# Kernel tuning notes

Hardware: AMD Instinct MI355X
Metric: run time of the kernel (lower is better)

## Reference

```python
import jax, jax.numpy as jnp
import numpy as np

NU = 200000  # num_users
NI = 200000  # num_items
D = 128      # d_model
B = 4096     # interaction batch


def setup_inputs() -> dict:
    key = jax.random.key(0)
    ks = jax.random.split(key, 24)
    f = lambda k, s, sc=1.0: (jax.random.normal(k, s, dtype=jnp.float32) * sc)
    s = 1.0 / np.sqrt(D)
    return {
        "user_id": jax.random.randint(ks[0], (B,), 0, NU),
        "prev_item_id": jax.random.randint(ks[1], (B,), 0, NI),
        "item_id": jax.random.randint(ks[2], (B,), 0, NI),
        "time_since_prev_item": jax.random.uniform(ks[3], (B, 1), dtype=jnp.float32),
        "time_since_prev_user": jax.random.uniform(ks[4], (B, 1), dtype=jnp.float32),
        "dynamic_user_emb": f(ks[5], (NU, D), 0.1),
        "dynamic_item_emb": f(ks[6], (NI, D), 0.1),
        "is_user_new": jnp.ones((NU, 1), dtype=jnp.float32),
        "is_item_new": jnp.ones((NI, 1), dtype=jnp.float32),
        "static_user_W": f(ks[7], (NU, D)),
        "static_item_W": f(ks[8], (NI, D)),
        "initial_user_emb": f(ks[9], (1, D)),
        "initial_item_emb": f(ks[10], (1, D)),
        "user_Wih": f(ks[11], (D, D + 1), s),
        "user_Whh": f(ks[12], (D, D), s),
        "user_bih": f(ks[13], (D,), s),
        "user_bhh": f(ks[14], (D,), s),
        "item_Wih": f(ks[15], (D, D + 1), s),
        "item_Whh": f(ks[16], (D, D), s),
        "item_bih": f(ks[17], (D,), s),
        "item_bhh": f(ks[18], (D,), s),
        "pred_W": f(ks[19], (2 * D, 4 * D), 1.0 / np.sqrt(4 * D)),
        "pred_b": f(ks[20], (2 * D,), 1.0 / np.sqrt(4 * D)),
        "td_W": f(ks[21], (D, 1)),
        "td_b": f(ks[22], (D,)),
    }


def _rnn_cell(x, h, Wih, Whh, bih, bhh):
    # torch.nn.RNNCell: tanh(x @ Wih^T + bih + h @ Whh^T + bhh)
    return jnp.tanh(x @ Wih.T + bih + h @ Whh.T + bhh)


def reference(user_id, prev_item_id, item_id, time_since_prev_item, time_since_prev_user,
              dynamic_user_emb, dynamic_item_emb, is_user_new, is_item_new,
              static_user_W, static_item_W, initial_user_emb, initial_item_emb,
              user_Wih, user_Whh, user_bih, user_bhh,
              item_Wih, item_Whh, item_bih, item_bhh,
              pred_W, pred_b, td_W, td_b):
    # gather dynamic embeddings (fall back to initial emb for new entities)
    user_emb = is_user_new[user_id] * initial_user_emb + dynamic_user_emb[user_id]
    item_emb = is_item_new[item_id] * initial_item_emb + dynamic_item_emb[item_id]
    prev_item_emb = is_item_new[prev_item_id] * initial_item_emb + dynamic_item_emb[prev_item_id]
    static_user_emb = static_user_W[user_id]
    static_item_emb = static_item_W[item_id]
    prev_static_item_emb = static_item_W[prev_item_id]

    # time projection + prediction head
    user_proj = user_emb * (1.0 + time_since_prev_item @ td_W.T + td_b)
    item_pred = jnp.concatenate(
        [user_proj, prev_item_emb, prev_static_item_emb, static_user_emb], axis=1) @ pred_W.T + pred_b
    item_target = jnp.concatenate([item_emb, static_item_emb], axis=1)

    # RNNCell updates
    updated_user_emb = _rnn_cell(jnp.concatenate([item_emb, time_since_prev_item], axis=1),
                                 user_emb, user_Wih, user_Whh, user_bih, user_bhh)
    updated_item_emb = _rnn_cell(jnp.concatenate([user_emb, time_since_prev_user], axis=1),
                                 item_emb, item_Wih, item_Whh, item_bih, item_bhh)

    # scatter back into persistent buffers (detached, as in torch)
    new_dyn_user = dynamic_user_emb.at[user_id].set(jax.lax.stop_gradient(updated_user_emb))
    new_dyn_item = dynamic_item_emb.at[item_id].set(jax.lax.stop_gradient(updated_item_emb))
    new_is_user_new = is_user_new.at[user_id].set(0.0)
    new_is_item_new = is_item_new.at[item_id].set(0.0)

    return (item_pred, item_target, updated_user_emb, user_emb, updated_item_emb, item_emb,
            new_dyn_user, new_dyn_item, new_is_user_new, new_is_item_new)
```

## Files before the change

kernel.cpp:

```cpp
#include <hip/hip_runtime.h>
#include <hip/hip_bf16.h>

#define NU 200000
#define NI 200000
#define D 128
#define BATCH 4096

typedef __bf16 bf16x8 __attribute__((ext_vector_type(8)));
typedef float f32x4 __attribute__((ext_vector_type(4)));

__global__ __launch_bounds__(256) void prep_kernel(
    const float* __restrict__ predW,
    const float* __restrict__ uWih, const float* __restrict__ uWhh,
    const float* __restrict__ iWih, const float* __restrict__ iWhh,
    const float* __restrict__ ubih, const float* __restrict__ ubhh,
    const float* __restrict__ ibih, const float* __restrict__ ibhh,
    const int* __restrict__ uid, const int* __restrict__ iid,
    __hip_bfloat16* __restrict__ wPred,
    __hip_bfloat16* __restrict__ wU, __hip_bfloat16* __restrict__ wI,
    float* __restrict__ biasU, float* __restrict__ biasI,
    int* __restrict__ lastU, int* __restrict__ lastI)
{
    int idx = blockIdx.x * 256 + threadIdx.x;
    if (idx < 131072) {
        wPred[idx] = __float2bfloat16(predW[idx]);
        return;
    }
    idx -= 131072;
    if (idx < 73728) {
        int z = idx / 36864;
        int r = idx - z * 36864;
        int j = r / 288, k = r - (r / 288) * 288;
        const float* Wih = z ? iWih : uWih;
        const float* Whh = z ? iWhh : uWhh;
        float v = 0.0f;
        if (k < 129)      v = Wih[j * 129 + k];
        else if (k < 257) v = Whh[j * 128 + (k - 129)];
        __hip_bfloat16* W = z ? wI : wU;
        W[j * 288 + k] = __float2bfloat16(v);
        return;
    }
    idx -= 73728;
    if (idx < 128) { biasU[idx] = ubih[idx] + ubhh[idx]; return; }
    idx -= 128;
    if (idx < 128) { biasI[idx] = ibih[idx] + ibhh[idx]; return; }
    idx -= 128;
    if (idx < BATCH) { atomicMax(&lastU[uid[idx]], idx); return; }
    idx -= BATCH;
    if (idx < BATCH) { atomicMax(&lastI[iid[idx]], idx); return; }
}

__global__ __launch_bounds__(128) void gather_kernel(
    const int* __restrict__ uid, const int* __restrict__ pid,
    const int* __restrict__ iid,
    const float* __restrict__ t_i, const float* __restrict__ t_u,
    const float* __restrict__ dynU, const float* __restrict__ dynI,
    const float* __restrict__ isU, const float* __restrict__ isI,
    const float* __restrict__ statU, const float* __restrict__ statI,
    const float* __restrict__ initU, const float* __restrict__ initI,
    const float* __restrict__ tdW, const float* __restrict__ tdb,
    float* __restrict__ o_user_emb, float* __restrict__ o_item_emb,
    float* __restrict__ o_target,
    __hip_bfloat16* __restrict__ xpred,
    __hip_bfloat16* __restrict__ xhU, __hip_bfloat16* __restrict__ xhI)
{
    int b = blockIdx.x;
    int d = threadIdx.x;
    int u = uid[b], i = iid[b], p = pid[b];
    float fu = isU[u], fi = isI[i], fp = isI[p];
    float iu = initU[d], ii = initI[d];
    float ue = fu * iu + dynU[(size_t)u * D + d];
    float ie = fi * ii + dynI[(size_t)i * D + d];
    float pe = fp * ii + dynI[(size_t)p * D + d];
    float su = statU[(size_t)u * D + d];
    float si = statI[(size_t)i * D + d];
    float sp = statI[(size_t)p * D + d];
    float ti = t_i[b], tu = t_u[b];

    o_user_emb[b * D + d] = ue;
    o_item_emb[b * D + d] = ie;
    o_target[b * 256 + d] = ie;
    o_target[b * 256 + 128 + d] = si;

    float proj = ue * (1.0f + ti * tdW[d] + tdb[d]);

    __hip_bfloat16* xp = xpred + (size_t)b * 512;
    xp[d]       = __float2bfloat16(proj);
    xp[128 + d] = __float2bfloat16(pe);
    xp[256 + d] = __float2bfloat16(sp);
    xp[384 + d] = __float2bfloat16(su);

    __hip_bfloat16* xu = xhU + (size_t)b * 288;
    xu[d]       = __float2bfloat16(ie);
    xu[129 + d] = __float2bfloat16(ue);
    __hip_bfloat16* xi = xhI + (size_t)b * 288;
    xi[d]       = __float2bfloat16(ue);
    xi[129 + d] = __float2bfloat16(ie);
    if (d == 0) {
        xu[128] = __float2bfloat16(ti);
        xi[128] = __float2bfloat16(tu);
    }
    if (d < 31) {
        xu[257 + d] = __float2bfloat16(0.0f);
        xi[257 + d] = __float2bfloat16(0.0f);
    }
}

__global__ __launch_bounds__(256) void gemm_pred(
    const __hip_bfloat16* __restrict__ A,
    const __hip_bfloat16* __restrict__ W,
    const float* __restrict__ bias,
    float* __restrict__ out)
{
    const int K = 512;
    int m0 = blockIdx.x * 64;
    int n0 = blockIdx.y * 64;
    int tid = threadIdx.x;
    int wave = tid >> 6;
    int lane = tid & 63;
    int quad = lane >> 4;
    int l15 = lane & 15;
    int row_a = m0 + wave * 16 + l15;

    f32x4 acc[4] = {};
    const __hip_bfloat16* Arow = A + (size_t)row_a * K;
    for (int k0 = 0; k0 < K; k0 += 32) {
        bf16x8 a = *reinterpret_cast<const bf16x8*>(Arow + k0 + quad * 8);
#pragma unroll
        for (int ct = 0; ct < 4; ++ct) {
            int rw = n0 + ct * 16 + l15;
            bf16x8 bb = *reinterpret_cast<const bf16x8*>(W + (size_t)rw * K + k0 + quad * 8);
            acc[ct] = __builtin_amdgcn_mfma_f32_16x16x32_bf16(a, bb, acc[ct], 0, 0, 0);
        }
    }
    int orow = m0 + wave * 16 + quad * 4;
#pragma unroll
    for (int ct = 0; ct < 4; ++ct) {
        int col = n0 + ct * 16 + l15;
        float bcol = bias[col];
#pragma unroll
        for (int r = 0; r < 4; ++r) {
            out[(size_t)(orow + r) * 256 + col] = acc[ct][r] + bcol;
        }
    }
}

__global__ __launch_bounds__(256) void gemm_cell(
    const __hip_bfloat16* __restrict__ A0, const __hip_bfloat16* __restrict__ A1,
    const __hip_bfloat16* __restrict__ W0, const __hip_bfloat16* __restrict__ W1,
    const float* __restrict__ b0, const float* __restrict__ b1,
    const int* __restrict__ ids0, const int* __restrict__ ids1,
    const int* __restrict__ last0, const int* __restrict__ last1,
    float* __restrict__ outB0, float* __restrict__ outB1,
    float* __restrict__ outD0, float* __restrict__ outD1)
{
    const int K = 288;
    int z = blockIdx.z;
    const __hip_bfloat16* A = z ? A1 : A0;
    const __hip_bfloat16* W = z ? W1 : W0;
    const float* bias = z ? b1 : b0;
    const int* ids  = z ? ids1 : ids0;
    const int* last = z ? last1 : last0;
    float* outB = z ? outB1 : outB0;
    float* outD = z ? outD1 : outD0;

    int m0 = blockIdx.x * 64;
    int n0 = blockIdx.y * 64;
    int tid = threadIdx.x;
    int wave = tid >> 6;
    int lane = tid & 63;
    int quad = lane >> 4;
    int l15 = lane & 15;
    int row_a = m0 + wave * 16 + l15;

    f32x4 acc[4] = {};
    const __hip_bfloat16* Arow = A + (size_t)row_a * K;
    for (int k0 = 0; k0 < K; k0 += 32) {
        bf16x8 a = *reinterpret_cast<const bf16x8*>(Arow + k0 + quad * 8);
#pragma unroll
        for (int ct = 0; ct < 4; ++ct) {
            int rw = n0 + ct * 16 + l15;
            bf16x8 bb = *reinterpret_cast<const bf16x8*>(W + (size_t)rw * K + k0 + quad * 8);
            acc[ct] = __builtin_amdgcn_mfma_f32_16x16x32_bf16(a, bb, acc[ct], 0, 0, 0);
        }
    }
    int orow = m0 + wave * 16 + quad * 4;
#pragma unroll
    for (int ct = 0; ct < 4; ++ct) {
        int col = n0 + ct * 16 + l15;
        float bcol = bias[col];
#pragma unroll
        for (int r = 0; r < 4; ++r) {
            int row = orow + r;
            float v = tanhf(acc[ct][r] + bcol);
            outB[(size_t)row * D + col] = v;
            int id = ids[row];
            if (last[id] == row) {
                outD[(size_t)id * D + col] = v;
            }
        }
    }
}

__global__ __launch_bounds__(256) void copy_kernel(
    const float4* __restrict__ dynU, const float4* __restrict__ dynI,
    const float* __restrict__ isU, const float* __restrict__ isI,
    const int* __restrict__ lastU, const int* __restrict__ lastI,
    float4* __restrict__ oDynU, float4* __restrict__ oDynI,
    float* __restrict__ oIsU, float* __restrict__ oIsI)
{
    long long idx = (long long)blockIdx.x * 256 + threadIdx.x;
    const long long NU4 = (long long)NU * 32;
    const long long NI4 = (long long)NI * 32;
    if (idx < NU4) {
        int row = (int)(idx >> 5);
        if (lastU[row] < 0) oDynU[idx] = dynU[idx];
        return;
    }
    idx -= NU4;
    if (idx < NI4) {
        int row = (int)(idx >> 5);
        if (lastI[row] < 0) oDynI[idx] = dynI[idx];
        return;
    }
    idx -= NI4;
    if (idx < NU) { oIsU[idx] = (lastU[idx] >= 0) ? 0.0f : isU[idx]; return; }
    idx -= NU;
    if (idx < NI) { oIsI[idx] = (lastI[idx] >= 0) ? 0.0f : isI[idx]; return; }
}

extern "C" void kernel_launch(void* const* d_in, const int* in_sizes, int n_in,
                              void* d_out, int out_size, void* d_ws, size_t ws_size,
                              hipStream_t stream) {
    const int*   uid   = (const int*)d_in[0];
    const int*   pid   = (const int*)d_in[1];
    const int*   iid   = (const int*)d_in[2];
    const float* t_i   = (const float*)d_in[3];
    const float* t_u   = (const float*)d_in[4];
    const float* dynU  = (const float*)d_in[5];
    const float* dynI  = (const float*)d_in[6];
    const float* isU   = (const float*)d_in[7];
    const float* isI   = (const float*)d_in[8];
    const float* statU = (const float*)d_in[9];
    const float* statI = (const float*)d_in[10];
    const float* initU = (const float*)d_in[11];
    const float* initI = (const float*)d_in[12];
    const float* uWih  = (const float*)d_in[13];
    const float* uWhh  = (const float*)d_in[14];
    const float* ubih  = (const float*)d_in[15];
    const float* ubhh  = (const float*)d_in[16];
    const float* iWih  = (const float*)d_in[17];
    const float* iWhh  = (const float*)d_in[18];
    const float* ibih  = (const float*)d_in[19];
    const float* ibhh  = (const float*)d_in[20];
    const float* predW = (const float*)d_in[21];
    const float* predb = (const float*)d_in[22];
    const float* tdW   = (const float*)d_in[23];
    const float* tdb   = (const float*)d_in[24];

    float* out = (float*)d_out;
    float* o_pred     = out;
    float* o_target   = out + 1048576;
    float* o_updU     = out + 2097152;
    float* o_userEmb  = out + 2621440;
    float* o_updI     = out + 3145728;
    float* o_itemEmb  = out + 3670016;
    float* o_dynU     = out + 4194304;
    float* o_dynI     = out + 29794304;
    float* o_isU      = out + 55394304;
    float* o_isI      = out + 55594304;

    char* ws = (char*)d_ws;
    int* lastU = (int*)ws;
    int* lastI = lastU + NU;
    __hip_bfloat16* xpred = (__hip_bfloat16*)(ws + 1600000);
    __hip_bfloat16* xhU   = (__hip_bfloat16*)(ws + 5794304);
    __hip_bfloat16* xhI   = (__hip_bfloat16*)(ws + 8153600);
    __hip_bfloat16* wPred = (__hip_bfloat16*)(ws + 10512896);
    __hip_bfloat16* wU    = (__hip_bfloat16*)(ws + 10775040);
    __hip_bfloat16* wI    = (__hip_bfloat16*)(ws + 10848768);
    float* biasU = (float*)(ws + 10922496);
    float* biasI = (float*)(ws + 10923008);

    hipMemsetAsync(lastU, 0xFF, (size_t)(NU + NI) * sizeof(int), stream);

    {
        int total = 131072 + 73728 + 256 + 2 * BATCH;
        int blocks = (total + 255) / 256;
        prep_kernel<<<blocks, 256, 0, stream>>>(
            predW, uWih, uWhh, iWih, iWhh, ubih, ubhh, ibih, ibhh,
            uid, iid, wPred, wU, wI, biasU, biasI, lastU, lastI);
    }

    gather_kernel<<<BATCH, 128, 0, stream>>>(
        uid, pid, iid, t_i, t_u, dynU, dynI, isU, isI, statU, statI,
        initU, initI, tdW, tdb, o_userEmb, o_itemEmb, o_target,
        xpred, xhU, xhI);

    gemm_pred<<<dim3(BATCH / 64, 4), 256, 0, stream>>>(xpred, wPred, predb, o_pred);

    gemm_cell<<<dim3(BATCH / 64, 2, 2), 256, 0, stream>>>(
        xhU, xhI, wU, wI, biasU, biasI, uid, iid, lastU, lastI,
        o_updU, o_updI, o_dynU, o_dynI);

    {
        long long total = (long long)NU * 32 + (long long)NI * 32 + NU + NI;
        int blocks = (int)((total + 255) / 256);
        copy_kernel<<<blocks, 256, 0, stream>>>(
            (const float4*)dynU, (const float4*)dynI, isU, isI, lastU, lastI,
            (float4*)o_dynU, (float4*)o_dynI, o_isU, o_isI);
    }
}
```

Baseline: 504.0 us.

## Fuse gather with unconditional table copy and merge GEMMs, scatter after copy

The full dynamic-embedding and is_new table copy now happens unconditionally inside the vectorized gather kernel, with no per-row lastU/lastI check. The two GEMM kernels merge into one launch that scatters updated rows and zeroes the is_new flags after the copy has finished. This cuts two launches and the dependent reads of the last-index arrays during the large copy. The gather now uses float4 loads and packed bf16 stores, and the cell input layout is reordered (h first, then x and time) so the vector stores stay aligned. The risk is that the scattered rows are written twice, and correctness relies on stream ordering between the copy and the GEMM.

```diff
diff --git a/kernel.cpp b/kernel.cpp
--- a/kernel.cpp
+++ b/kernel.cpp
@@ -8,6 +8,20 @@
 
 typedef __bf16 bf16x8 __attribute__((ext_vector_type(8)));
 typedef float f32x4 __attribute__((ext_vector_type(4)));
+
+__device__ __forceinline__ void store_bf16x4(__hip_bfloat16* p, float4 v) {
+    union { __hip_bfloat16 h[4]; uint2 u; } pk;
+    pk.h[0] = __float2bfloat16(v.x);
+    pk.h[1] = __float2bfloat16(v.y);
+    pk.h[2] = __float2bfloat16(v.z);
+    pk.h[3] = __float2bfloat16(v.w);
+    *reinterpret_cast<uint2*>(p) = pk.u;
+}
+
+__device__ __forceinline__ float4 f4_fma(float s, float4 a, float4 b) {
+    return make_float4(fmaf(s, a.x, b.x), fmaf(s, a.y, b.y),
+                       fmaf(s, a.z, b.z), fmaf(s, a.w, b.w));
+}
 
 __global__ __launch_bounds__(256) void prep_kernel(
     const float* __restrict__ predW,
@@ -34,8 +48,8 @@
         const float* Wih = z ? iWih : uWih;
         const float* Whh = z ? iWhh : uWhh;
         float v = 0.0f;
-        if (k < 129)      v = Wih[j * 129 + k];
-        else if (k < 257) v = Whh[j * 128 + (k - 129)];
+        if (k < 128)      v = Whh[j * 128 + k];
+        else if (k < 257) v = Wih[j * 129 + (k - 128)];
         __hip_bfloat16* W = z ? wI : wU;
         W[j * 288 + k] = __float2bfloat16(v);
         return;
@@ -50,7 +64,7 @@
     if (idx < BATCH) { atomicMax(&lastI[iid[idx]], idx); return; }
 }
 
-__global__ __launch_bounds__(128) void gather_kernel(
+__global__ __launch_bounds__(256) void gather_copy_kernel(
     const int* __restrict__ uid, const int* __restrict__ pid,
     const int* __restrict__ iid,
     const float* __restrict__ t_i, const float* __restrict__ t_u,
@@ -62,171 +76,162 @@
     float* __restrict__ o_user_emb, float* __restrict__ o_item_emb,
     float* __restrict__ o_target,
     __hip_bfloat16* __restrict__ xpred,
-    __hip_bfloat16* __restrict__ xhU, __hip_bfloat16* __restrict__ xhI)
+    __hip_bfloat16* __restrict__ xhU, __hip_bfloat16* __restrict__ xhI,
+    float4* __restrict__ oDynU, float4* __restrict__ oDynI,
+    float4* __restrict__ oIsU, float4* __restrict__ oIsI)
 {
-    int b = blockIdx.x;
-    int d = threadIdx.x;
-    int u = uid[b], i = iid[b], p = pid[b];
-    float fu = isU[u], fi = isI[i], fp = isI[p];
-    float iu = initU[d], ii = initI[d];
-    float ue = fu * iu + dynU[(size_t)u * D + d];
-    float ie = fi * ii + dynI[(size_t)i * D + d];
-    float pe = fp * ii + dynI[(size_t)p * D + d];
-    float su = statU[(size_t)u * D + d];
-    float si = statI[(size_t)i * D + d];
-    float sp = statI[(size_t)p * D + d];
-    float ti = t_i[b], tu = t_u[b];
-
-    o_user_emb[b * D + d] = ue;
-    o_item_emb[b * D + d] = ie;
-    o_target[b * 256 + d] = ie;
-    o_target[b * 256 + 128 + d] = si;
-
-    float proj = ue * (1.0f + ti * tdW[d] + tdb[d]);
-
-    __hip_bfloat16* xp = xpred + (size_t)b * 512;
-    xp[d]       = __float2bfloat16(proj);
-    xp[128 + d] = __float2bfloat16(pe);
-    xp[256 + d] = __float2bfloat16(sp);
-    xp[384 + d] = __float2bfloat16(su);
-
-    __hip_bfloat16* xu = xhU + (size_t)b * 288;
-    xu[d]       = __float2bfloat16(ie);
-    xu[129 + d] = __float2bfloat16(ue);
-    __hip_bfloat16* xi = xhI + (size_t)b * 288;
-    xi[d]       = __float2bfloat16(ue);
-    xi[129 + d] = __float2bfloat16(ie);
-    if (d == 0) {
-        xu[128] = __float2bfloat16(ti);
-        xi[128] = __float2bfloat16(tu);
+    long long idx = (long long)blockIdx.x * 256 + threadIdx.x;
+    if (idx < 131072) {
+        int b = (int)(idx >> 5);
+        int g = (int)(idx & 31);
+        const float4* dU4 = (const float4*)dynU;
+        const float4* dI4 = (const float4*)dynI;
+        const float4* sU4 = (const float4*)statU;
+        const float4* sI4 = (const float4*)statI;
+
+        int u = uid[b], i = iid[b], p = pid[b];
+        float fu = isU[u], fi = isI[i], fp = isI[p];
+        float ti = t_i[b], tu = t_u[b];
+
+        float4 iu = ((const float4*)initU)[g];
+        float4 ii = ((const float4*)initI)[g];
+        float4 ue = f4_fma(fu, iu, dU4[(size_t)u * 32 + g]);
+        float4 ie = f4_fma(fi, ii, dI4[(size_t)i * 32 + g]);
+        float4 pe = f4_fma(fp, ii, dI4[(size_t)p * 32 + g]);
+        float4 su = sU4[(size_t)u * 32 + g];
+        float4 si = sI4[(size_t)i * 32 + g];
+        float4 sp = sI4[(size_t)p * 32 + g];
+        float4 tw = ((const float4*)tdW)[g];
+        float4 tb = ((const float4*)tdb)[g];
+
+        ((float4*)o_user_emb)[(size_t)b * 32 + g] = ue;
+        ((float4*)o_item_emb)[(size_t)b * 32 + g] = ie;
+        ((float4*)o_target)[(size_t)b * 64 + g] = ie;
+        ((float4*)o_target)[(size_t)b * 64 + 32 + g] = si;
+
+        float4 f = f4_fma(ti, tw, tb);
+        float4 proj = make_float4(ue.x * (1.0f + f.x), ue.y * (1.0f + f.y),
+                                  ue.z * (1.0f + f.z), ue.w * (1.0f + f.w));
+
+        __hip_bfloat16* xp = xpred + (size_t)b * 512;
+        store_bf16x4(xp + 4 * g, proj);
+        store_bf16x4(xp + 128 + 4 * g, pe);
+        store_bf16x4(xp + 256 + 4 * g, sp);
+        store_bf16x4(xp + 384 + 4 * g, su);
+
+        __hip_bfloat16* xu = xhU + (size_t)b * 288;
+        store_bf16x4(xu + 4 * g, ue);
+        store_bf16x4(xu + 128 + 4 * g, ie);
+        __hip_bfloat16* xi = xhI + (size_t)b * 288;
+        store_bf16x4(xi + 4 * g, ie);
+        store_bf16x4(xi + 128 + 4 * g, ue);
+        if (g < 8) {
+            float4 zu = make_float4(g == 0 ? ti : 0.0f, 0.0f, 0.0f, 0.0f);
+            float4 zi = make_float4(g == 0 ? tu : 0.0f, 0.0f, 0.0f, 0.0f);
+            store_bf16x4(xu + 256 + 4 * g, zu);
+            store_bf16x4(xi + 256 + 4 * g, zi);
+        }
+        return;
     }
-    if (d < 31) {
-        xu[257 + d] = __float2bfloat16(0.0f);
-        xi[257 + d] = __float2bfloat16(0.0f);
-    }
-}
-
-__global__ __launch_bounds__(256) void gemm_pred(
-    const __hip_bfloat16* __restrict__ A,
-    const __hip_bfloat16* __restrict__ W,
-    const float* __restrict__ bias,
-    float* __restrict__ out)
+    idx -= 131072;
+    if (idx < 6400000) { oDynU[idx] = ((const float4*)dynU)[idx]; return; }
+    idx -= 6400000;
+    if (idx < 6400000) { oDynI[idx] = ((const float4*)dynI)[idx]; return; }
+    idx -= 6400000;
+    if (idx < 50000) { oIsU[idx] = ((const float4*)isU)[idx]; return; }
+    idx -= 50000;
+    if (idx < 50000) { oIsI[idx] = ((const float4*)isI)[idx]; return; }
+}
+
+__global__ __launch_bounds__(256) void gemm_fused(
+    const __hip_bfloat16* __restrict__ xpred,
+    const __hip_bfloat16* __restrict__ wPred,
+    const float* __restrict__ predb, float* __restrict__ o_pred,
+    const __hip_bfloat16* __restrict__ xhU, const __hip_bfloat16* __restrict__ xhI,
+    const __hip_bfloat16* __restrict__ wU, const __hip_bfloat16* __restrict__ wI,
+    const float* __restrict__ biasU, const float* __restrict__ biasI,
+    const int* __restrict__ uid, const int* __restrict__ iid,
+    const int* __restrict__ lastU, const int* __restrict__ lastI,
+    float* __restrict__ o_updU, float* __restrict__ o_updI,
+    float* __restrict__ o_dynU, float* __restrict__ o_dynI,
+    float* __restrict__ o_isU, float* __restrict__ o_isI)
 {
-    const int K = 512;
-    int m0 = blockIdx.x * 64;
-    int n0 = blockIdx.y * 64;
+    int bx = blockIdx.x;
     int tid = threadIdx.x;
-    int wave = tid >> 6;
-    int lane = tid & 63;
-    int quad = lane >> 4;
-    int l15 = lane & 15;
-    int row_a = m0 + wave * 16 + l15;
-
-    f32x4 acc[4] = {};
-    const __hip_bfloat16* Arow = A + (size_t)row_a * K;
-    for (int k0 = 0; k0 < K; k0 += 32) {
-        bf16x8 a = *reinterpret_cast<const bf16x8*>(Arow + k0 + quad * 8);
+    int wave = tid >> 6, lane = tid & 63, quad = lane >> 4, l15 = lane & 15;
+
+    if (bx < 256) {
+        const int K = 512;
+        int m0 = (bx & 63) * 64, n0 = (bx >> 6) * 64;
+        f32x4 acc[4] = {};
+        const __hip_bfloat16* Arow = xpred + (size_t)(m0 + wave * 16 + l15) * K;
+        for (int k0 = 0; k0 < K; k0 += 32) {
+            bf16x8 a = *reinterpret_cast<const bf16x8*>(Arow + k0 + quad * 8);
+#pragma unroll
+            for (int ct = 0; ct < 4; ++ct) {
+                bf16x8 b = *reinterpret_cast<const bf16x8*>(
+                    wPred + (size_t)(n0 + ct * 16 + l15) * K + k0 + quad * 8);
+                acc[ct] = __builtin_amdgcn_mfma_f32_16x16x32_bf16(a, b, acc[ct], 0, 0, 0);
+            }
+        }
+        int orow = m0 + wave * 16 + quad * 4;
 #pragma unroll
         for (int ct = 0; ct < 4; ++ct) {
-            int rw = n0 + ct * 16 + l15;
-            bf16x8 bb = *reinterpret_cast<const bf16x8*>(W + (size_t)rw * K + k0 + quad * 8);
-            acc[ct] = __builtin_amdgcn_mfma_f32_16x16x32_bf16(a, bb, acc[ct], 0, 0, 0);
-        }
-    }
-    int orow = m0 + wave * 16 + quad * 4;
-#pragma unroll
-    for (int ct = 0; ct < 4; ++ct) {
-        int col = n0 + ct * 16 + l15;
-        float bcol = bias[col];
-#pragma unroll
-        for (int r = 0; r < 4; ++r) {
-            out[(size_t)(orow + r) * 256 + col] = acc[ct][r] + bcol;
-        }
-    }
-}
-
-__global__ __launch_bounds__(256) void gemm_cell(
-    const __hip_bfloat16* __restrict__ A0, const __hip_bfloat16* __restrict__ A1,
-    const __hip_bfloat16* __restrict__ W0, const __hip_bfloat16* __restrict__ W1,
-    const float* __restrict__ b0, const float* __restrict__ b1,
-    const int* __restrict__ ids0, const int* __restrict__ ids1,
-    const int* __restrict__ last0, const int* __restrict__ last1,
-    float* __restrict__ outB0, float* __restrict__ outB1,
-    float* __restrict__ outD0, float* __restrict__ outD1)
-{
-    const int K = 288;
-    int z = blockIdx.z;
-    const __hip_bfloat16* A = z ? A1 : A0;
-    const __hip_bfloat16* W = z ? W1 : W0;
-    const float* bias = z ? b1 : b0;
-    const int* ids  = z ? ids1 : ids0;
-    const int* last = z ? last1 : last0;
-    float* outB = z ? outB1 : outB0;
-    float* outD = z ? outD1 : outD0;
-
-    int m0 = blockIdx.x * 64;
-    int n0 = blockIdx.y * 64;
-    int tid = threadIdx.x;
-    int wave = tid >> 6;
-    int lane = tid & 63;
-    int quad = lane >> 4;
-    int l15 = lane & 15;
-    int row_a = m0 + wave * 16 + l15;
-
-    f32x4 acc[4] = {};
-    const __hip_bfloat16* Arow = A + (size_t)row_a * K;
-    for (int k0 = 0; k0 < K; k0 += 32) {
-        bf16x8 a = *reinterpret_cast<const bf16x8*>(Arow + k0 + quad * 8);
-#pragma unroll
-        for (int ct = 0; ct < 4; ++ct) {
-            int rw = n0 + ct * 16 + l15;
-            bf16x8 bb = *reinterpret_cast<const bf16x8*>(W + (size_t)rw * K + k0 + quad * 8);
-            acc[ct] = __builtin_amdgcn_mfma_f32_16x16x32_bf16(a, bb, acc[ct], 0, 0, 0);
-        }
-    }
-    int orow = m0 + wave * 16 + quad * 4;
-#pragma unroll
-    for (int ct = 0; ct < 4; ++ct) {
-        int col = n0 + ct * 16 + l15;
-        float bcol = bias[col];
+            int col = n0 + ct * 16 + l15;
+            float bc = predb[col];
+#pragma unroll
+            for (int r = 0; r < 4; ++r)
+                o_pred[(size_t)(orow + r) * 256 + col] = acc[ct][r] + bc;
+        }
+    } else {
+        bx -= 256;
+        int z = bx >> 7; bx &= 127;
+        int m0 = (bx & 63) * 64, n0 = (bx >> 6) * 64;
+        const __hip_bfloat16* A = z ? xhI : xhU;
+        const __hip_bfloat16* W = z ? wI : wU;
+        const float* bias = z ? biasI : biasU;
+        const int* ids  = z ? iid : uid;
+        const int* last = z ? lastI : lastU;
+        float* outB = z ? o_updI : o_updU;
+        float* outD = z ? o_dynI : o_dynU;
+        float* oIs  = z ? o_isI  : o_isU;
+
+        const int K = 288;
+        f32x4 acc[4] = {};
+        const __hip_bfloat16* Arow = A + (size_t)(m0 + wave * 16 + l15) * K;
+        for (int k0 = 0; k0 < K; k0 += 32) {
+            bf16x8 a = *reinterpret_cast<const bf16x8*>(Arow + k0 + quad * 8);
+#pragma unroll
+            for (int ct = 0; ct < 4; ++ct) {
+                bf16x8 b = *reinterpret_cast<const bf16x8*>(
+                    W + (size_t)(n0 + ct * 16 + l15) * K + k0 + quad * 8);
+                acc[ct] = __builtin_amdgcn_mfma_f32_16x16x32_bf16(a, b, acc[ct], 0, 0, 0);
+            }
+        }
+        int orow = m0 + wave * 16 + quad * 4;
+        int rid[4], win[4];
 #pragma unroll
         for (int r = 0; r < 4; ++r) {
             int row = orow + r;
-            float v = tanhf(acc[ct][r] + bcol);
-            outB[(size_t)row * D + col] = v;
-            int id = ids[row];
-            if (last[id] == row) {
-                outD[(size_t)id * D + col] = v;
+            rid[r] = ids[row];
+            win[r] = (last[rid[r]] == row);
+        }
+#pragma unroll
+        for (int ct = 0; ct < 4; ++ct) {
+            int col = n0 + ct * 16 + l15;
+            float bc = bias[col];
+#pragma unroll
+            for (int r = 0; r < 4; ++r) {
+                float v = tanhf(acc[ct][r] + bc);
+                outB[(size_t)(orow + r) * D + col] = v;
+                if (win[r]) outD[(size_t)rid[r] * D + col] = v;
             }
         }
+        if (n0 == 0 && l15 == 0) {
+#pragma unroll
+            for (int r = 0; r < 4; ++r) oIs[rid[r]] = 0.0f;
+        }
     }
-}
-
-__global__ __launch_bounds__(256) void copy_kernel(
-    const float4* __restrict__ dynU, const float4* __restrict__ dynI,
-    const float* __restrict__ isU, const float* __restrict__ isI,
-    const int* __restrict__ lastU, const int* __restrict__ lastI,
-    float4* __restrict__ oDynU, float4* __restrict__ oDynI,
-    float* __restrict__ oIsU, float* __restrict__ oIsI)
-{
-    long long idx = (long long)blockIdx.x * 256 + threadIdx.x;
-    const long long NU4 = (long long)NU * 32;
-    const long long NI4 = (long long)NI * 32;
-    if (idx < NU4) {
-        int row = (int)(idx >> 5);
-        if (lastU[row] < 0) oDynU[idx] = dynU[idx];
-        return;
-    }
-    idx -= NU4;
-    if (idx < NI4) {
-        int row = (int)(idx >> 5);
-        if (lastI[row] < 0) oDynI[idx] = dynI[idx];
-        return;
-    }
-    idx -= NI4;
-    if (idx < NU) { oIsU[idx] = (lastU[idx] >= 0) ? 0.0f : isU[idx]; return; }
-    idx -= NU;
-    if (idx < NI) { oIsI[idx] = (lastI[idx] >= 0) ? 0.0f : isI[idx]; return; }
 }
 
 extern "C" void kernel_launch(void* const* d_in, const int* in_sizes, int n_in,
@@ -284,30 +289,19 @@
 
     hipMemsetAsync(lastU, 0xFF, (size_t)(NU + NI) * sizeof(int), stream);
 
-    {
-        int total = 131072 + 73728 + 256 + 2 * BATCH;
-        int blocks = (total + 255) / 256;
-        prep_kernel<<<blocks, 256, 0, stream>>>(
-            predW, uWih, uWhh, iWih, iWhh, ubih, ubhh, ibih, ibhh,
-            uid, iid, wPred, wU, wI, biasU, biasI, lastU, lastI);
-    }
-
-    gather_kernel<<<BATCH, 128, 0, stream>>>(
+    prep_kernel<<<833, 256, 0, stream>>>(
+        predW, uWih, uWhh, iWih, iWhh, ubih, ubhh, ibih, ibhh,
+        uid, iid, wPred, wU, wI, biasU, biasI, lastU, lastI);
+
+    gather_copy_kernel<<<50903, 256, 0, stream>>>(
         uid, pid, iid, t_i, t_u, dynU, dynI, isU, isI, statU, statI,
         initU, initI, tdW, tdb, o_userEmb, o_itemEmb, o_target,
-        xpred, xhU, xhI);
-
-    gemm_pred<<<dim3(BATCH / 64, 4), 256, 0, stream>>>(xpred, wPred, predb, o_pred);
-
-    gemm_cell<<<dim3(BATCH / 64, 2, 2), 256, 0, stream>>>(
-        xhU, xhI, wU, wI, biasU, biasI, uid, iid, lastU, lastI,
-        o_updU, o_updI, o_dynU, o_dynI);
-
-    {
-        long long total = (long long)NU * 32 + (long long)NI * 32 + NU + NI;
-        int blocks = (int)((total + 255) / 256);
-        copy_kernel<<<blocks, 256, 0, stream>>>(
-            (const float4*)dynU, (const float4*)dynI, isU, isI, lastU, lastI,
-            (float4*)o_dynU, (float4*)o_dynI, o_isU, o_isI);
-    }
-}
+        xpred, xhU, xhI,
+        (float4*)o_dynU, (float4*)o_dynI, (float4*)o_isU, (float4*)o_isI);
+
+    gemm_fused<<<512, 256, 0, stream>>>(
+        xpred, wPred, predb, o_pred,
+        xhU, xhI, wU, wI, biasU, biasI,
+        uid, iid, lastU, lastI,
+        o_updU, o_updI, o_dynU, o_dynI, o_isU, o_isI);
+}
```

Result: no change. 498.3 us (-1.1%).
